# Kernel optimization log

Hardware: AMD Instinct MI355X
Metric: run time of the kernel (lower is better)

Reference implementation:

```python
import jax, jax.numpy as jnp
import numpy as np

D = 512; N_HEAD = 8; D_HEAD = 64; D_INNER = 2048; SEG = 512; N_LAYER = 2; BATCH = 32
NUM_ITEMS = 50000
OMEGA = [2, 3, 4, 5, 7, 11, 21, 50]  # len == N_HEAD, required by multi-scale mask broadcast
EPS = 1e-8
STD = 0.02


def _layer_norm(x, w, b):
    mu = x.mean(-1, keepdims=True)
    var = ((x - mu) ** 2).mean(-1, keepdims=True)
    return (x - mu) / jnp.sqrt(var + EPS) * w + b


def _masks():
    # dir_mask: triu(ones, 1) (reverse=False); ms_mask[i,j,m] per omega band
    dir_mask = jnp.triu(jnp.ones((SEG, SEG), jnp.float32), 1)
    ms = np.stack([np.tri(SEG, SEG, o - 1) != np.tri(SEG, SEG, -o) for o in OMEGA], axis=-1)
    return dir_mask, jnp.asarray(ms)


def _pos_emb():
    freq = jnp.arange(0, D, 2, dtype=jnp.float32)
    inv_freq = 1.0 / jnp.power(10000.0, freq / D)
    pos_seq = jnp.arange(SEG, -SEG, -1.0, dtype=jnp.float32)  # length 2*SEG
    sinusoid = pos_seq[:, None] * inv_freq[None, :]
    return jnp.concatenate([jnp.sin(sinusoid), jnp.cos(sinusoid)], axis=-1)  # (2S, D)


def _rel_shift_bnij(x, klen):
    b, n, i, j2 = x.shape
    x = x.reshape(b, n, j2, i)[:, :, 1:, :].reshape(b, n, i, j2 - 1)
    return x[:, :, :, :klen]


def setup_inputs() -> dict:
    key = jax.random.key(0)
    ks = jax.random.split(key, 16)
    L = N_LAYER
    item_emb = STD * jax.random.normal(ks[0], (NUM_ITEMS + 1, D), jnp.float32)
    item_emb = item_emb.at[0].set(0.0)  # padding_idx=0
    proj = lambda k: STD * jax.random.normal(k, (L, D, N_HEAD, D_HEAD), jnp.float32)
    return {
        "input_ids": jax.random.randint(ks[1], (BATCH, SEG), 0, NUM_ITEMS + 1),
        "input_mask": jnp.zeros((BATCH, SEG), jnp.float32),
        "item_emb": item_emb,
        "Wq": proj(ks[2]), "Wk": proj(ks[3]), "Wv": proj(ks[4]),
        "Wr": proj(ks[5]), "Wo": proj(ks[6]),
        "r_r_bias": STD * jax.random.normal(ks[7], (L, N_HEAD, D_HEAD), jnp.float32),
        "r_w_bias": STD * jax.random.normal(ks[8], (L, N_HEAD, D_HEAD), jnp.float32),
        "ln_attn_w": jnp.ones((L, D), jnp.float32), "ln_attn_b": jnp.zeros((L, D), jnp.float32),
        "W1": STD * jax.random.normal(ks[9], (L, D, D_INNER), jnp.float32),
        "b1": jnp.zeros((L, D_INNER), jnp.float32),
        "W2": STD * jax.random.normal(ks[10], (L, D_INNER, D), jnp.float32),
        "b2": jnp.zeros((L, D), jnp.float32),
        "ln_ff_w": jnp.ones((L, D), jnp.float32), "ln_ff_b": jnp.zeros((L, D), jnp.float32),
    }


def reference(input_ids, input_mask, item_emb, Wq, Wk, Wv, Wr, Wo, r_r_bias, r_w_bias,
              ln_attn_w, ln_attn_b, W1, b1, W2, b2, ln_ff_w, ln_ff_b):
    ids = input_ids.T                      # (S, B)
    im = input_mask.T.astype(jnp.float32)  # (S, B)
    dir_mask, ms_mask = _masks()
    # data_mask: (q,k,b); attn_mask: (q,k,b,n) via multi-scale bands (training path)
    data_mask = im[None, :, :] + im[:, None, :] + dir_mask[:, :, None]
    attn_mask = ((data_mask[:, :, :, None] + (~ms_mask)[:, :, None, :].astype(jnp.float32)) > 0).astype(jnp.float32)
    mask_bnij = jnp.transpose(attn_mask, (2, 3, 0, 1))  # (b,n,i,j)

    h = item_emb[ids]          # (S, B, D)
    pos = _pos_emb()           # (2S, D), shared across batch
    scale = 1.0 / np.sqrt(D_HEAD).astype(np.float32)

    for l in range(N_LAYER):
        k_h = jnp.einsum('ibh,hnd->ibnd', h, Wk[l])
        v_h = jnp.einsum('ibh,hnd->ibnd', h, Wv[l])
        k_r = jnp.einsum('jh,hnd->jnd', pos, Wr[l])   # pos shared across batch
        q_h = jnp.einsum('ibh,hnd->ibnd', h, Wq[l])
        ac = jnp.einsum('ibnd,jbnd->bnij', q_h + r_w_bias[l], k_h)
        bd = jnp.einsum('ibnd,jnd->bnij', q_h + r_r_bias[l], k_r)
        bd = _rel_shift_bnij(bd, SEG)
        attn_score = (ac + bd) * scale - 1e30 * mask_bnij
        attn_prob = jax.nn.softmax(attn_score, axis=3)
        attn_vec = jnp.einsum('bnij,jbnd->ibnd', attn_prob, v_h)
        attn_out = jnp.einsum('ibnd,hnd->ibh', attn_vec, Wo[l])
        h = _layer_norm(attn_out + h, ln_attn_w[l], ln_attn_b[l])
        ff = jax.nn.gelu(h @ W1[l] + b1[l], approximate=False) @ W2[l] + b2[l]
        h = _layer_norm(ff + h, ln_ff_w[l], ln_ff_b[l])

    return jnp.transpose(h, (1, 0, 2))  # (B, S, D)
```

## Files before the change

### kernel.cpp

```cpp
#include <hip/hip_runtime.h>
#include <math.h>


#define S_  512
#define B_  32
#define D_  512
#define NH  8
#define DH  64
#define DI  2048
#define M_  (S_*B_)
#define QKV_LD 1536
#define WL  3407872
#define FP32_ONE 0x3F800000u

typedef unsigned short ushort_t;
typedef __attribute__((ext_vector_type(8))) short short8;
typedef __attribute__((ext_vector_type(4))) float f32x4;

__constant__ int OMEGA_C[8] = {2, 3, 4, 5, 7, 11, 21, 50};

__device__ __forceinline__ float b2f(ushort_t us) {
    return __uint_as_float(((unsigned int)us) << 16);
}
__device__ __forceinline__ ushort_t f2b(float f) {
    unsigned int u = __float_as_uint(f);
    return (ushort_t)((u + 0x7fffu + ((u >> 16) & 1u)) >> 16);
}
__device__ __forceinline__ float ldx(const void* p, size_t idx, bool isbf) {
    return isbf ? b2f(((const ushort_t*)p)[idx]) : ((const float*)p)[idx];
}
__device__ __forceinline__ void async16(const ushort_t* g, ushort_t* l) {
    __builtin_amdgcn_global_load_lds(
        (const __attribute__((address_space(1))) unsigned int*)g,
        (__attribute__((address_space(3))) unsigned int*)l, 16, 0, 0);
}

__device__ __forceinline__ float fast_gelu(float v) {
    float x  = v * 0.7071067811865475f;
    float ax = fabsf(x);
    float t  = __builtin_amdgcn_rcpf(fmaf(0.3275911f, ax, 1.f));
    float p  = fmaf(fmaf(fmaf(fmaf(1.061405429f, t, -1.453152027f),
                              t, 1.421413741f),
                         t, -0.284496736f),
                    t, 0.254829592f) * t;
    float e    = __expf(-ax * ax);
    float erfa = fmaf(-p, e, 1.f);
    float erfx = copysignf(erfa, x);
    return 0.5f * v * (1.f + erfx);
}

#define DPPA(v, ctrl) v += __int_as_float(__builtin_amdgcn_update_dpp(0, __float_as_int(v), ctrl, 0xf, 0xf, true))
__device__ __forceinline__ void dpp_sum64(float& v) {
    DPPA(v, 0x111); DPPA(v, 0x112); DPPA(v, 0x114);
    DPPA(v, 0x118); DPPA(v, 0x142); DPPA(v, 0x143);
}
#define DPPROR(v, ctrl) __int_as_float(__builtin_amdgcn_update_dpp(__float_as_int(v), __float_as_int(v), ctrl, 0xf, 0xf, false))
__device__ __forceinline__ float row16_sum(float v) {
    v += DPPROR(v, 0x128); v += DPPROR(v, 0x124);
    v += DPPROR(v, 0x122); v += DPPROR(v, 0x121);
    return v;
}
__device__ __forceinline__ float row16_max(float v) {
    v = fmaxf(v, DPPROR(v, 0x128)); v = fmaxf(v, DPPROR(v, 0x124));
    v = fmaxf(v, DPPROR(v, 0x122)); v = fmaxf(v, DPPROR(v, 0x121));
    return v;
}
__device__ __forceinline__ float rlane(float v, int l) {
    return __int_as_float(__builtin_amdgcn_readlane(__float_as_int(v), l));
}

__global__ __launch_bounds__(256) void embed_kernel(const int* __restrict__ ids,
                                                    const void* __restrict__ emb,
                                                    ushort_t* __restrict__ h,
                                                    const unsigned int* __restrict__ dtp) {
    const bool isbf = (dtp[0] != FP32_ONE);
    int idx = blockIdx.x * 256 + threadIdx.x;
    int d8 = idx & 63;
    int row = idx >> 6;
    int s = row >> 5, b = row & 31;
    int id = ids[b * S_ + s];
    size_t src = (size_t)id * D_ + d8 * 8;
    if (isbf) {
        *(uint4*)(h + (size_t)row * D_ + d8 * 8) = *(const uint4*)((const ushort_t*)emb + src);
    } else {
        const float* e = (const float*)emb + src;
        float4 a0 = ((const float4*)e)[0], a1 = ((const float4*)e)[1];
        uint4 pk;
        pk.x = (unsigned)f2b(a0.x) | ((unsigned)f2b(a0.y) << 16);
        pk.y = (unsigned)f2b(a0.z) | ((unsigned)f2b(a0.w) << 16);
        pk.z = (unsigned)f2b(a1.x) | ((unsigned)f2b(a1.y) << 16);
        pk.w = (unsigned)f2b(a1.z) | ((unsigned)f2b(a1.w) << 16);
        *(uint4*)(h + (size_t)row * D_ + d8 * 8) = pk;
    }
}

__global__ __launch_bounds__(256) void posemb_kernel(ushort_t* __restrict__ pos) {
    int flat = blockIdx.x * 256 + threadIdx.x;
    int p = flat >> 8, k = flat & 255;
    float inv = expf((float)k * -0.035977892078031f);
    float val = (512.0f - (float)p) * inv;
    pos[p * D_ + k]       = f2b(sinf(val));
    pos[p * D_ + 256 + k] = f2b(cosf(val));
}

__global__ __launch_bounds__(256) void transp_cvt4(
    const void* __restrict__ s0, const void* __restrict__ s1,
    const void* __restrict__ s2, const void* __restrict__ s3,
    ushort_t* __restrict__ wbuf, const unsigned int* __restrict__ dtp) {
    const bool isbf = (dtp[0] != FP32_ONE);
    __shared__ float tt[32][33];
    int z = blockIdx.z, layer = z >> 2, t4 = z & 3;
    const void* srcs[4] = {s0, s1, s2, s3};
    const void* in = srcs[t4];
    size_t inoff = (size_t)layer * 262144;
    ushort_t* out = wbuf + (size_t)layer * WL + (size_t)t4 * 262144;
    int tx = threadIdx.x & 31, ty = threadIdx.x >> 5;
    int n0 = blockIdx.x * 32, k0 = blockIdx.y * 32;
#pragma unroll
    for (int it = 0; it < 4; ++it)
        tt[ty + it * 8][tx] = ldx(in, inoff + (size_t)(k0 + ty + it * 8) * 512 + n0 + tx, isbf);
    __syncthreads();
#pragma unroll
    for (int it = 0; it < 4; ++it)
        out[(size_t)(n0 + ty + it * 8) * 512 + k0 + tx] = f2b(tt[tx][ty + it * 8]);
}

__global__ __launch_bounds__(256) void transp_cvtL(const void* __restrict__ in, size_t perlin,
                                                   ushort_t* __restrict__ wbuf, size_t outoff,
                                                   const unsigned int* __restrict__ dtp,
                                                   int K, int N) {
    const bool isbf = (dtp[0] != FP32_ONE);
    __shared__ float tt[32][33];
    int layer = blockIdx.z;
    size_t inoff = (size_t)layer * perlin;
    ushort_t* out = wbuf + (size_t)layer * WL + outoff;
    int tx = threadIdx.x & 31, ty = threadIdx.x >> 5;
    int n0 = blockIdx.x * 32, k0 = blockIdx.y * 32;
#pragma unroll
    for (int it = 0; it < 4; ++it)
        tt[ty + it * 8][tx] = ldx(in, inoff + (size_t)(k0 + ty + it * 8) * N + n0 + tx, isbf);
    __syncthreads();
#pragma unroll
    for (int it = 0; it < 4; ++it)
        out[(size_t)(n0 + ty + it * 8) * K + k0 + tx] = f2b(tt[tx][ty + it * 8]);
}

__global__ __launch_bounds__(256) void cvtL(const void* __restrict__ in, size_t perlin,
                                            ushort_t* __restrict__ wbuf, size_t outoff,
                                            const unsigned int* __restrict__ dtp, int nelem) {
    const bool isbf = (dtp[0] != FP32_ONE);
    int layer = blockIdx.z;
    int i = blockIdx.x * 256 + threadIdx.x;
    if (i < nelem)
        wbuf[(size_t)layer * WL + outoff + i] = f2b(ldx(in, (size_t)layer * perlin + i, isbf));
}

template<int EPI>
__global__ __launch_bounds__(256)
void mfma_gemm(const ushort_t* __restrict__ A, int lda,
               const ushort_t* __restrict__ Bt, int ldb,
               const void* __restrict__ biasv, size_t biasoff,
               ushort_t* __restrict__ C, int ldc,
               const unsigned int* __restrict__ dtp, int M, int N, int K) {
    const bool isbf = (dtp[0] != FP32_ONE);
    __shared__ ushort_t As[128 * 32];
    __shared__ ushort_t Bs[128 * 32];
    const int tid = threadIdx.x;
    const int nwg = gridDim.x * gridDim.y;
    const int wg  = blockIdx.y * gridDim.x + blockIdx.x;
    const int cpx = nwg >> 3;
    const int swz = (wg & 7) * cpx + (wg >> 3);
    const int bm = (swz / gridDim.y) * 128;
    const int bn = (swz % gridDim.y) * 128;
    const int w = tid >> 6, lane = tid & 63;
    const int wr = w >> 1, wc = w & 1;
    const int quad = lane >> 4, l16 = lane & 15;
    const int rsub = lane >> 2;
    const int kcg  = (lane & 3) ^ ((rsub >> 1) & 3);
    const int fsw  = (l16 >> 1) & 3;

    f32x4 acc[4][4];
#pragma unroll
    for (int i = 0; i < 4; ++i)
#pragma unroll
        for (int j = 0; j < 4; ++j)
#pragma unroll
            for (int r = 0; r < 4; ++r) acc[i][j][r] = 0.f;

    for (int k0 = 0; k0 < K; k0 += 32) {
#pragma unroll
        for (int c = 0; c < 2; ++c) {
            int grp = c * 4 + w;
            int row = grp * 16 + rsub;
            async16(A  + (size_t)(bm + row) * lda + k0 + kcg * 8, As + grp * 512);
            async16(Bt + (size_t)(bn + row) * ldb + k0 + kcg * 8, Bs + grp * 512);
        }
        __syncthreads();

        short8 af[4], bf[4];
#pragma unroll
        for (int t = 0; t < 4; ++t) {
            int ra = wr * 64 + t * 16 + l16;
            int rb = wc * 64 + t * 16 + l16;
            af[t] = *(const short8*)(As + ra * 32 + ((quad ^ fsw) * 8));
            bf[t] = *(const short8*)(Bs + rb * 32 + ((quad ^ fsw) * 8));
        }
#pragma unroll
        for (int tr = 0; tr < 4; ++tr)
#pragma unroll
            for (int tc = 0; tc < 4; ++tc)
                acc[tr][tc] = __builtin_amdgcn_mfma_f32_16x16x32_bf16(bf[tc], af[tr], acc[tr][tc], 0, 0, 0);
        __syncthreads();
    }

    float bv[4][4];
    if (EPI >= 1) {
#pragma unroll
        for (int tc = 0; tc < 4; ++tc)
#pragma unroll
            for (int r = 0; r < 4; ++r)
                bv[tc][r] = ldx(biasv, biasoff + bn + wc * 64 + tc * 16 + quad * 4 + r, isbf);
    }
#pragma unroll
    for (int tr = 0; tr < 4; ++tr) {
        int grow = bm + wr * 64 + tr * 16 + l16;
#pragma unroll
        for (int tc = 0; tc < 4; ++tc) {
            int gcb = bn + wc * 64 + tc * 16 + quad * 4;
            float x[4];
#pragma unroll
            for (int r = 0; r < 4; ++r) {
                float v = acc[tr][tc][r];
                if (EPI >= 1) v += bv[tc][r];
                if (EPI == 2) v = fast_gelu(v);
                x[r] = v;
            }
            uint2 pk;
            pk.x = (unsigned)f2b(x[0]) | ((unsigned)f2b(x[1]) << 16);
            pk.y = (unsigned)f2b(x[2]) | ((unsigned)f2b(x[3]) << 16);
            *(uint2*)(C + (size_t)grow * ldc + gcb) = pk;
        }
    }
}

__global__ __launch_bounds__(256) void attn_mfma(
    ushort_t* __restrict__ qkv, const ushort_t* __restrict__ krb,
    const void* __restrict__ rwb, const void* __restrict__ rrb, size_t boff,
    const void* __restrict__ im,
    const unsigned int* __restrict__ dtp) {
    const bool isbf = (dtp[0] != FP32_ONE);
    __shared__ ushort_t Ks[128 * 64];
    __shared__ ushort_t VT[64 * 128];
    __shared__ ushort_t Rs[64 * 64];
    __shared__ float    BD2[4 * 16 * 64];
    __shared__ ushort_t Ps[4 * 16 * 128];
    __shared__ float    imk[128];
    __shared__ float    imq[64];

    const int tid = threadIdx.x;
    const int i0 = blockIdx.x * 64;
    const int b  = blockIdx.y;
    const int n  = blockIdx.z;
    const int o  = OMEGA_C[n];
    const int noff = n * DH;
    const int j0 = i0 - 64;
    const int w = tid >> 6, lane = tid & 63;
    const int quad = lane >> 4, l16 = lane & 15;

#pragma unroll
    for (int it = 0; it < 4; ++it) {
        int q4 = it * 256 + tid;
        int c  = q4 >> 3, ch = q4 & 7;
        int jc = j0 + c; jc = jc < 0 ? 0 : jc;
        size_t rowb = (size_t)(jc * B_ + b) * QKV_LD + noff;
        *(uint4*)(Ks + c * 64 + ((ch ^ (c & 7)) << 3)) = *(const uint4*)(qkv + rowb + 512 + ch * 8);
        ushort_t v8[8];
        *(uint4*)v8 = *(const uint4*)(qkv + rowb + 1024 + ch * 8);
#pragma unroll
        for (int e = 0; e < 8; ++e) {
            int vr = ch * 8 + e;
            VT[vr * 128 + (((c >> 3) ^ (vr & 15)) << 3) + (c & 7)] = v8[e];
        }
    }
#pragma unroll
    for (int it = 0; it < 2; ++it) {
        int q4 = it * 256 + tid;
        int m = q4 >> 3, ch = q4 & 7;
        *(uint4*)(Rs + m * 64 + ((ch ^ (m & 7)) << 3)) =
            *(const uint4*)(krb + (size_t)(512 - m) * 512 + noff + ch * 8);
    }
    if (tid < 128) {
        int j = j0 + tid;
        imk[tid] = (j >= 0) ? ldx(im, b * S_ + j, isbf) : 0.f;
    } else if (tid < 192) {
        imq[tid - 128] = ldx(im, b * S_ + i0 + (tid - 128), isbf);
    }
    __syncthreads();

    const int qrow = i0 + w * 16 + l16;
    size_t qbase = (size_t)(qrow * B_ + b) * QKV_LD + noff;
    short8 aw[2], ar[2];
#pragma unroll
    for (int kc = 0; kc < 2; ++kc) {
        int kof = kc * 32 + quad * 8;
        ushort_t qe[8];
        *(uint4*)qe = *(const uint4*)(qkv + qbase + kof);
#pragma unroll
        for (int e = 0; e < 8; ++e) {
            float f = b2f(qe[e]);
            ((ushort_t*)&aw[kc])[e] = f2b(f + ldx(rwb, boff + noff + kof + e, isbf));
            ((ushort_t*)&ar[kc])[e] = f2b(f + ldx(rrb, boff + noff + kof + e, isbf));
        }
    }

    f32x4 accs[8];
#pragma unroll
    for (int ct = 0; ct < 8; ++ct) {
        int kr = ct * 16 + l16;
        short8 b0 = *(const short8*)(Ks + kr * 64 + ((quad ^ (kr & 7)) << 3));
        short8 b1 = *(const short8*)(Ks + kr * 64 + (((quad + 4) ^ (kr & 7)) << 3));
        f32x4 z = {0.f, 0.f, 0.f, 0.f};
        z = __builtin_amdgcn_mfma_f32_16x16x32_bf16(aw[0], b0, z, 0, 0, 0);
        z = __builtin_amdgcn_mfma_f32_16x16x32_bf16(aw[1], b1, z, 0, 0, 0);
        accs[ct] = z;
    }
    float* BD2w = BD2 + w * 16 * 64;
#pragma unroll
    for (int mt = 0; mt < 4; ++mt) {
        int rr = mt * 16 + l16;
        short8 b0 = *(const short8*)(Rs + rr * 64 + ((quad ^ (rr & 7)) << 3));
        short8 b1 = *(const short8*)(Rs + rr * 64 + (((quad + 4) ^ (rr & 7)) << 3));
        f32x4 z = {0.f, 0.f, 0.f, 0.f};
        z = __builtin_amdgcn_mfma_f32_16x16x32_bf16(ar[0], b0, z, 0, 0, 0);
        z = __builtin_amdgcn_mfma_f32_16x16x32_bf16(ar[1], b1, z, 0, 0, 0);
#pragma unroll
        for (int r = 0; r < 4; ++r)
            BD2w[(quad * 4 + r) * 64 + mt * 16 + l16] = z[r];
    }

    float im_i[4];
#pragma unroll
    for (int r = 0; r < 4; ++r) im_i[r] = imq[w * 16 + quad * 4 + r];

    float sc[8][4];
#pragma unroll
    for (int ct = 0; ct < 8; ++ct) {
        int cl = ct * 16 + l16;
        float imk_c = imk[cl];
#pragma unroll
        for (int r = 0; r < 4; ++r) {
            int qrl = w * 16 + quad * 4 + r;
            int rel = qrl + 64 - cl;
            int relc = rel < 0 ? 0 : (rel > 63 ? 63 : rel);
            float bd = BD2w[(quad * 4 + r) * 64 + relc];
            bool valid = (rel >= 0) && (rel < o) && (rel <= i0 + qrl)
                         && (im_i[r] + imk_c <= 0.f);
            sc[ct][r] = valid ? (accs[ct][r] + bd) * 0.125f : -1e30f;
        }
    }
    float rl[4];
#pragma unroll
    for (int r = 0; r < 4; ++r) {
        float mx = sc[0][r];
#pragma unroll
        for (int ct = 1; ct < 8; ++ct) mx = fmaxf(mx, sc[ct][r]);
        mx = row16_max(mx);
        float l = 0.f;
#pragma unroll
        for (int ct = 0; ct < 8; ++ct) {
            float pv = __expf(sc[ct][r] - mx);
            sc[ct][r] = pv;
            l += pv;
        }
        l = row16_sum(l);
        rl[r] = 1.f / l;
    }
    ushort_t* Pw = Ps + w * 16 * 128;
#pragma unroll
    for (int ct = 0; ct < 8; ++ct)
#pragma unroll
        for (int r = 0; r < 4; ++r) {
            int prow = quad * 4 + r;
            Pw[prow * 128 + ((((ct * 2 + (l16 >> 3)) ^ prow) & 15) << 3) + (l16 & 7)]
                = f2b(sc[ct][r] * rl[r]);
        }

    short8 aP[4];
#pragma unroll
    for (int kc = 0; kc < 4; ++kc)
        aP[kc] = *(const short8*)(Pw + l16 * 128 + ((((kc * 4 + quad) ^ l16) & 15) << 3));

    const int qg = i0 + w * 16 + l16;
    const size_t obase = (size_t)(qg * B_ + b) * QKV_LD + noff;
#pragma unroll
    for (int dt = 0; dt < 4; ++dt) {
        f32x4 accT = {0.f, 0.f, 0.f, 0.f};
#pragma unroll
        for (int kc = 0; kc < 4; ++kc) {
            int vrow = dt * 16 + l16;
            short8 bV = *(const short8*)(VT + vrow * 128 + ((((kc * 4 + quad) ^ (vrow & 15)) & 15) << 3));
            accT = __builtin_amdgcn_mfma_f32_16x16x32_bf16(bV, aP[kc], accT, 0, 0, 0);
        }
        uint2 pk;
        pk.x = (unsigned)f2b(accT[0]) | ((unsigned)f2b(accT[1]) << 16);
        pk.y = (unsigned)f2b(accT[2]) | ((unsigned)f2b(accT[3]) << 16);
        *(uint2*)(qkv + obase + dt * 16 + quad * 4) = pk;
    }
}

__global__ __launch_bounds__(256) void add_ln_kernel(
    const ushort_t* __restrict__ x, ushort_t* __restrict__ h,
    const void* __restrict__ w, const void* __restrict__ b, size_t boff,
    const unsigned int* __restrict__ dtp) {
    const bool isbf = (dtp[0] != FP32_ONE);
    int lane = threadIdx.x & 63;
    int row = blockIdx.x * 4 + (threadIdx.x >> 6);
    size_t base = (size_t)row * D_ + lane * 8;
    ushort_t xe[8], he[8];
    *(uint4*)xe = *(const uint4*)(x + base);
    *(uint4*)he = *(const uint4*)(h + base);
    float v[8];
    float s = 0.f, ss = 0.f;
#pragma unroll
    for (int e = 0; e < 8; ++e) {
        v[e] = b2f(xe[e]) + b2f(he[e]);
        s += v[e]; ss += v[e] * v[e];
    }
    dpp_sum64(s); dpp_sum64(ss);
    float S = rlane(s, 63), SS = rlane(ss, 63);
    float mu  = S * (1.f / D_);
    float var = fmaxf(SS * (1.f / D_) - mu * mu, 0.f);
    float inv = rsqrtf(var + 1e-8f);
    ushort_t oe[8];
#pragma unroll
    for (int e = 0; e < 8; ++e)
        oe[e] = f2b((v[e] - mu) * inv * ldx(w, boff + lane * 8 + e, isbf)
                    + ldx(b, boff + lane * 8 + e, isbf));
    *(uint4*)(h + base) = *(uint4*)oe;
}

__global__ __launch_bounds__(256) void writeout_kernel(const ushort_t* __restrict__ h,
                                                       void* __restrict__ out,
                                                       const unsigned int* __restrict__ dtp) {
    const bool isbf = (dtp[0] != FP32_ONE);
    int idx = blockIdx.x * 256 + threadIdx.x;
    int d8 = idx & 63;
    int rest = idx >> 6;
    int s = rest & (S_ - 1), b = rest >> 9;
    ushort_t ve[8];
    *(uint4*)ve = *(const uint4*)(h + ((size_t)(s * B_ + b) << 9) + d8 * 8);
    if (isbf) {
        *(uint4*)((ushort_t*)out + (size_t)idx * 8) = *(uint4*)ve;
    } else {
        float* op = (float*)out + (size_t)idx * 8;
        ((float4*)op)[0] = make_float4(b2f(ve[0]), b2f(ve[1]), b2f(ve[2]), b2f(ve[3]));
        ((float4*)op)[1] = make_float4(b2f(ve[4]), b2f(ve[5]), b2f(ve[6]), b2f(ve[7]));
    }
}

extern "C" void kernel_launch(void* const* d_in, const int* in_sizes, int n_in,
                              void* d_out, int out_size, void* d_ws, size_t ws_size,
                              hipStream_t stream) {
    (void)in_sizes; (void)n_in; (void)out_size; (void)ws_size;
    const int*  ids = (const int*)d_in[0];
    const void* im  = d_in[1];
    const void* emb = d_in[2];
    const void* Wq = d_in[3], *Wk = d_in[4], *Wv = d_in[5], *Wr = d_in[6], *Wo = d_in[7];
    const void* rrb = d_in[8], *rwb = d_in[9];
    const void* lnaw = d_in[10], *lnab = d_in[11];
    const void* W1 = d_in[12], *b1 = d_in[13], *W2 = d_in[14], *b2 = d_in[15];
    const void* lnfw = d_in[16], *lnfb = d_in[17];
    const unsigned int* dtp = (const unsigned int*)d_in[10];

    char* wsb = (char*)d_ws;
    ushort_t* h    = (ushort_t*)wsb;
    ushort_t* qkv  = (ushort_t*)(wsb + (16u << 20));
    ushort_t* tmp  = (ushort_t*)(wsb + (64u << 20));
    ushort_t* ff1  = (ushort_t*)(wsb + (80u << 20));
    ushort_t* wbuf = (ushort_t*)(wsb + (144u << 20));
    ushort_t* posb = (ushort_t*)(wsb + (157u << 20));
    ushort_t* krb0 = (ushort_t*)(wsb + (158u << 20));
    ushort_t* krb1 = (ushort_t*)(wsb + (159u << 20));

    embed_kernel<<<4096, 256, 0, stream>>>(ids, emb, h, dtp);
    posemb_kernel<<<1024, 256, 0, stream>>>(posb);

    transp_cvt4<<<dim3(16, 16, 8), 256, 0, stream>>>(Wq, Wk, Wv, Wr, wbuf, dtp);
    cvtL<<<dim3(1024, 1, 2), 256, 0, stream>>>(Wo, 262144, wbuf, 1048576, dtp, 262144);
    transp_cvtL<<<dim3(64, 16, 2), 256, 0, stream>>>(W1, 1048576, wbuf, 1310720, dtp, 512, 2048);
    transp_cvtL<<<dim3(16, 64, 2), 256, 0, stream>>>(W2, 1048576, wbuf, 2359296, dtp, 2048, 512);

    mfma_gemm<0><<<dim3(8, 4), 256, 0, stream>>>(posb, 512, wbuf + 786432, 512, nullptr, 0, krb0, 512, dtp, 1024, 512, 512);
    mfma_gemm<0><<<dim3(8, 4), 256, 0, stream>>>(posb, 512, wbuf + WL + 786432, 512, nullptr, 0, krb1, 512, dtp, 1024, 512, 512);

    for (int l = 0; l < 2; ++l) {
        size_t boff = (size_t)l * 512;
        size_t b1off = (size_t)l * 2048;
        ushort_t* qkvT = wbuf + (size_t)l * WL;
        ushort_t* woc  = qkvT + 1048576;
        ushort_t* w1T  = woc  + 262144;
        ushort_t* w2T  = w1T  + 1048576;
        ushort_t* krb  = l ? krb1 : krb0;

        mfma_gemm<0><<<dim3(128, 12), 256, 0, stream>>>(h, 512, qkvT, 512, nullptr, 0, qkv, QKV_LD, dtp, M_, QKV_LD, 512);

        attn_mfma<<<dim3(8, 32, 8), 256, 0, stream>>>(qkv, krb, rwb, rrb, boff, im, dtp);

        mfma_gemm<0><<<dim3(128, 4), 256, 0, stream>>>(qkv, QKV_LD, woc, 512, nullptr, 0, tmp, 512, dtp, M_, 512, 512);
        add_ln_kernel<<<4096, 256, 0, stream>>>(tmp, h, lnaw, lnab, boff, dtp);

        mfma_gemm<2><<<dim3(128, 16), 256, 0, stream>>>(h, 512, w1T, 512, b1, b1off, ff1, DI, dtp, M_, DI, 512);
        mfma_gemm<1><<<dim3(128, 4),  256, 0, stream>>>(ff1, DI, w2T, 2048, b2, boff, tmp, 512, dtp, M_, 512, DI);
        add_ln_kernel<<<4096, 256, 0, stream>>>(tmp, h, lnfw, lnfb, boff, dtp);
    }

    writeout_kernel<<<4096, 256, 0, stream>>>(h, d_out, dtp);
}
```

Measured before the change: 801.3 us.

## Triple-buffer GEMM shared-memory tiles with async prefetch two stages ahead

The bf16 MFMA GEMM moves from a single shared-memory buffer with a full sync on every K step to a 3-stage ring of A/B tiles. Global-to-LDS async loads for tile t+2 are issued before computing tile t, and explicit vmcnt waits plus raw barriers replace __syncthreads. This is meant to hide global load latency behind the MFMA work. It triples the LDS footprint to 48KB per block, which may reduce occupancy, and it depends on the hand-written waitcnt counts being correct.

```diff
diff --git a/kernel.cpp b/kernel.cpp
--- a/kernel.cpp
+++ b/kernel.cpp
@@ -163,8 +163,8 @@
                ushort_t* __restrict__ C, int ldc,
                const unsigned int* __restrict__ dtp, int M, int N, int K) {
     const bool isbf = (dtp[0] != FP32_ONE);
-    __shared__ ushort_t As[128 * 32];
-    __shared__ ushort_t Bs[128 * 32];
+    __shared__ ushort_t As[3][128 * 32];
+    __shared__ ushort_t Bs[3][128 * 32];
     const int tid = threadIdx.x;
     const int nwg = gridDim.x * gridDim.y;
     const int wg  = blockIdx.y * gridDim.x + blockIdx.x;
@@ -179,6 +179,19 @@
     const int kcg  = (lane & 3) ^ ((rsub >> 1) & 3);
     const int fsw  = (l16 >> 1) & 3;
 
+    const ushort_t* ga0 = A  + (size_t)(bm + w * 16 + rsub) * lda + kcg * 8;
+    const ushort_t* ga1 = A  + (size_t)(bm + (4 + w) * 16 + rsub) * lda + kcg * 8;
+    const ushort_t* gb0 = Bt + (size_t)(bn + w * 16 + rsub) * ldb + kcg * 8;
+    const ushort_t* gb1 = Bt + (size_t)(bn + (4 + w) * 16 + rsub) * ldb + kcg * 8;
+
+#define STAGE_T(kt, bi) do {                                  \
+        int _k0 = (kt) << 5;                                  \
+        async16(ga0 + _k0, As[bi] + w * 512);                 \
+        async16(gb0 + _k0, Bs[bi] + w * 512);                 \
+        async16(ga1 + _k0, As[bi] + (4 + w) * 512);           \
+        async16(gb1 + _k0, Bs[bi] + (4 + w) * 512);           \
+    } while (0)
+
     f32x4 acc[4][4];
 #pragma unroll
     for (int i = 0; i < 4; ++i)
@@ -187,31 +200,42 @@
 #pragma unroll
             for (int r = 0; r < 4; ++r) acc[i][j][r] = 0.f;
 
-    for (int k0 = 0; k0 < K; k0 += 32) {
-#pragma unroll
-        for (int c = 0; c < 2; ++c) {
-            int grp = c * 4 + w;
-            int row = grp * 16 + rsub;
-            async16(A  + (size_t)(bm + row) * lda + k0 + kcg * 8, As + grp * 512);
-            async16(Bt + (size_t)(bn + row) * ldb + k0 + kcg * 8, Bs + grp * 512);
-        }
-        __syncthreads();
+    const int nt = K >> 5;
+    STAGE_T(0, 0);
+    STAGE_T(1, 1);
+    int cur = 0, nxt = 2;
+    for (int t = 0; t < nt; ++t) {
+        if (t + 2 < nt) {
+            STAGE_T(t + 2, nxt);
+            asm volatile("s_waitcnt vmcnt(8)" ::: "memory");
+        } else if (t + 1 < nt) {
+            asm volatile("s_waitcnt vmcnt(4)" ::: "memory");
+        } else {
+            asm volatile("s_waitcnt vmcnt(0)" ::: "memory");
+        }
+        __builtin_amdgcn_s_barrier();
+        asm volatile("" ::: "memory");
 
         short8 af[4], bf[4];
 #pragma unroll
-        for (int t = 0; t < 4; ++t) {
-            int ra = wr * 64 + t * 16 + l16;
-            int rb = wc * 64 + t * 16 + l16;
-            af[t] = *(const short8*)(As + ra * 32 + ((quad ^ fsw) * 8));
-            bf[t] = *(const short8*)(Bs + rb * 32 + ((quad ^ fsw) * 8));
+        for (int tt = 0; tt < 4; ++tt) {
+            int ra = wr * 64 + tt * 16 + l16;
+            int rb = wc * 64 + tt * 16 + l16;
+            af[tt] = *(const short8*)(As[cur] + ra * 32 + ((quad ^ fsw) * 8));
+            bf[tt] = *(const short8*)(Bs[cur] + rb * 32 + ((quad ^ fsw) * 8));
         }
 #pragma unroll
         for (int tr = 0; tr < 4; ++tr)
 #pragma unroll
             for (int tc = 0; tc < 4; ++tc)
                 acc[tr][tc] = __builtin_amdgcn_mfma_f32_16x16x32_bf16(bf[tc], af[tr], acc[tr][tc], 0, 0, 0);
-        __syncthreads();
-    }
+
+        asm volatile("s_waitcnt lgkmcnt(0)" ::: "memory");
+        __builtin_amdgcn_s_barrier();
+        cur = cur == 2 ? 0 : cur + 1;
+        nxt = nxt == 2 ? 0 : nxt + 1;
+    }
+#undef STAGE_T
 
     float bv[4][4];
     if (EPI >= 1) {
```

After: 762.5 us. 4.8% less time.
